# Kernel tuning notes

Hardware: AMD Instinct MI355X
Metric: run time of the kernel (lower is better)

Reference implementation:

```python
import jax, jax.numpy as jnp
import numpy as np

B, PIX_H, PIX_W = 64, 14, 14
ENC_D, DEC_D, ATT_D, EMB_D = 2048, 512, 512, 512
VOCAB, MAX_LEN = 10000, 52  # 51 decode steps


def setup_inputs() -> dict:
    key = jax.random.key(0)
    ks = jax.random.split(key, 24)
    s = 0.02
    inp = {
        'encoder_out': jax.random.normal(ks[0], (B, PIX_H, PIX_W, ENC_D), jnp.float32),
        'encoded_captions': jax.random.randint(ks[1], (B, MAX_LEN), 0, VOCAB),
        'caption_lengths': jnp.sort(jax.random.randint(ks[2], (B,), 2, MAX_LEN + 1))[::-1].at[0].set(MAX_LEN),
        # embedding (uniform -0.1..0.1 as in init_weights)
        'emb': jax.random.uniform(ks[3], (VOCAB, EMB_D), jnp.float32, -0.1, 0.1),
        # attention network
        'W_enc_att': jax.random.normal(ks[4], (ENC_D, ATT_D)) * s,
        'b_enc_att': jnp.zeros((ATT_D,)),
        'W_dec_att': jax.random.normal(ks[5], (DEC_D, ATT_D)) * s,
        'b_dec_att': jnp.zeros((ATT_D,)),
        'W_full_att': jax.random.normal(ks[6], (ATT_D, 1)) * s,
        'b_full_att': jnp.zeros((1,)),
        # init hidden state
        'W_init_h': jax.random.normal(ks[7], (ENC_D, DEC_D)) * s,
        'b_init_h': jnp.zeros((DEC_D,)),
        'W_init_c': jax.random.normal(ks[8], (ENC_D, DEC_D)) * s,
        'b_init_c': jnp.zeros((DEC_D,)),
        # gate
        'W_fbeta': jax.random.normal(ks[9], (DEC_D, ENC_D)) * s,
        'b_fbeta': jnp.zeros((ENC_D,)),
        # LSTMCell (torch gate order i,f,g,o)
        'W_ih': jax.random.normal(ks[10], (EMB_D + ENC_D, 4 * DEC_D)) * s,
        'W_hh': jax.random.normal(ks[11], (DEC_D, 4 * DEC_D)) * s,
        'b_ih': jnp.zeros((4 * DEC_D,)),
        'b_hh': jnp.zeros((4 * DEC_D,)),
        # fc (uniform -0.1..0.1, zero bias per init_weights)
        'W_fc': jax.random.uniform(ks[12], (DEC_D, VOCAB), jnp.float32, -0.1, 0.1),
        'b_fc': jnp.zeros((VOCAB,)),
    }
    return inp


def _decode(encoder_out, encoded_captions, caption_lengths, emb,
            W_enc_att, b_enc_att, W_dec_att, b_dec_att, W_full_att, b_full_att,
            W_init_h, b_init_h, W_init_c, b_init_c, W_fbeta, b_fbeta,
            W_ih, W_hh, b_ih, b_hh, W_fc, b_fc):
    bsz = encoder_out.shape[0]
    enc = encoder_out.reshape(bsz, -1, encoder_out.shape[-1])  # [B, P, ENC_D]
    embeddings = emb[encoded_captions]                          # [B, T+1, E]
    mean_enc = enc.mean(axis=1)
    h0 = mean_enc @ W_init_h + b_init_h
    c0 = mean_enc @ W_init_c + b_init_c
    att_enc = enc @ W_enc_att + b_enc_att                       # [B, P, A] precomputed
    T = encoded_captions.shape[1] - 1                           # max decode steps
    decode_len = caption_lengths - 1                            # [B]
    step_mask = jnp.arange(T)[:, None] < decode_len[None, :]    # [T, B]
    emb_seq = jnp.swapaxes(embeddings[:, :T, :], 0, 1)          # [T, B, E]

    def step(carry, xt):
        h, c = carry
        emb_t, m = xt                                           # [B,E], [B]
        # attention: 2 linears + tanh + softmax + weighted sum
        att_dec = h @ W_dec_att + b_dec_att                     # [B, A]
        e = (jnp.tanh(att_enc + att_dec[:, None, :]) @ W_full_att + b_full_att)[..., 0]  # [B, P]
        alpha = jax.nn.softmax(e, axis=-1)
        awe = jnp.einsum('bp,bpd->bd', alpha, enc)              # [B, ENC_D]
        gate = jax.nn.sigmoid(h @ W_fbeta + b_fbeta)
        awe = gate * awe
        # LSTMCell
        x = jnp.concatenate([emb_t, awe], axis=1)
        gates = x @ W_ih + h @ W_hh + (b_ih + b_hh)
        i, f, g, o = jnp.split(gates, 4, axis=1)
        c_new = jax.nn.sigmoid(f) * c + jax.nn.sigmoid(i) * jnp.tanh(g)
        h_new = jax.nn.sigmoid(o) * jnp.tanh(c_new)
        mm = m[:, None]
        h = jnp.where(mm, h_new, h)  # freeze finished rows (== batch_size_t slicing)
        c = jnp.where(mm, c_new, c)
        preds = (h @ W_fc + b_fc) * mm  # dropout = identity (eval mode)
        return (h, c), (preds, alpha * mm)

    (_, _), (preds_seq, alpha_seq) = jax.lax.scan(step, (h0, c0), (emb_seq, step_mask))
    predictions = jnp.swapaxes(preds_seq, 0, 1)  # [B, T, V]
    alphas = jnp.swapaxes(alpha_seq, 0, 1)       # [B, T, P]
    return predictions, alphas


def reference(encoder_out, encoded_captions, caption_lengths, emb,
              W_enc_att, b_enc_att, W_dec_att, b_dec_att, W_full_att, b_full_att,
              W_init_h, b_init_h, W_init_c, b_init_c, W_fbeta, b_fbeta,
              W_ih, W_hh, b_ih, b_hh, W_fc, b_fc):
    predictions, alphas = _decode(encoder_out, encoded_captions, caption_lengths, emb,
                                  W_enc_att, b_enc_att, W_dec_att, b_dec_att, W_full_att, b_full_att,
                                  W_init_h, b_init_h, W_init_c, b_init_c, W_fbeta, b_fbeta,
                                  W_ih, W_hh, b_ih, b_hh, W_fc, b_fc)
    return predictions, encoded_captions, caption_lengths - 1, alphas
```

## Files before the change

kernel.cpp:

```cpp
#include <hip/hip_runtime.h>
#include <hip/hip_bf16.h>
#include <math.h>

#define BB 64
#define NPIX 196
#define ENCD 2048
#define DECD 512
#define VOCAB_N 10000
#define MAXLEN 52
#define TT 51
#define NPADFC 10048

#define PRED_SZ   (BB * TT * VOCAB_N)
#define CAPS_SZ   (BB * MAXLEN)
#define LENS_SZ   (BB)
#define ALPHAS_OFF (PRED_SZ + CAPS_SZ + LENS_SZ)

typedef __attribute__((ext_vector_type(8))) short short8;
typedef __attribute__((ext_vector_type(4))) short short4v;
typedef __attribute__((ext_vector_type(4))) float f32x4;

__device__ __forceinline__ float fsigm(float x) {
    return 1.0f / (1.0f + __expf(-x));
}
__device__ __forceinline__ float ftanh(float x) {
    x = fminf(fmaxf(x, -15.0f), 15.0f);
    float e = __expf(2.0f * x);
    return (e - 1.0f) / (e + 1.0f);
}
__device__ __forceinline__ float bf2f(unsigned short u) {
    union { unsigned int i; float f; } v;
    v.i = ((unsigned int)u) << 16;
    return v.f;
}
__device__ __forceinline__ unsigned short f2bf(float f) {
    union { float f; unsigned int i; } v;
    v.f = f;
    unsigned int r = v.i + 0x7FFFu + ((v.i >> 16) & 1u);
    return (unsigned short)(r >> 16);
}

__global__ __launch_bounds__(256) void gemm_mfma(
    const unsigned short* __restrict__ A, int lda,
    const unsigned short* __restrict__ Wp, int Npad,
    int nkb, long slice_stride,
    float* __restrict__ C, unsigned short* __restrict__ C16, long ldc,
    const float* __restrict__ bias, int N, int act,
    const int* __restrict__ caplen, int t)
{
    const int n0 = blockIdx.x * 64;
    const int m0 = blockIdx.y * 64;
    const int kz = blockIdx.z;
    A  += (size_t)kz * nkb * 32;
    Wp += (size_t)kz * nkb * Npad * 32;
    if (C) C += (size_t)kz * slice_stride;

    const int w  = threadIdx.x >> 6;
    const int l  = threadIdx.x & 63;
    const int lr = l & 15;
    const int q  = l >> 4;

    const unsigned short* ap = A + (size_t)(m0 + 16 * w + lr) * lda + q * 8;
    const unsigned short* bp = Wp + (size_t)(n0 + lr) * 32 + q * 8;
    const size_t bstep = (size_t)Npad * 32;

    f32x4 acc[4];
#pragma unroll
    for (int i = 0; i < 4; ++i) acc[i] = (f32x4){0.f, 0.f, 0.f, 0.f};

    short8 a  = *(const short8*)ap;
    short8 b0 = *(const short8*)(bp);
    short8 b1 = *(const short8*)(bp + 512);
    short8 b2 = *(const short8*)(bp + 1024);
    short8 b3 = *(const short8*)(bp + 1536);

    for (int kb = 0; kb < nkb; ++kb) {
        const size_t nxt = (kb + 1 < nkb) ? 1 : 0;
        const unsigned short* apn = ap + nxt * 32;
        const unsigned short* bpn = bp + nxt * bstep;
        short8 an  = *(const short8*)apn;
        short8 bn0 = *(const short8*)(bpn);
        short8 bn1 = *(const short8*)(bpn + 512);
        short8 bn2 = *(const short8*)(bpn + 1024);
        short8 bn3 = *(const short8*)(bpn + 1536);
        acc[0] = __builtin_amdgcn_mfma_f32_16x16x32_bf16(a, b0, acc[0], 0, 0, 0);
        acc[1] = __builtin_amdgcn_mfma_f32_16x16x32_bf16(a, b1, acc[1], 0, 0, 0);
        acc[2] = __builtin_amdgcn_mfma_f32_16x16x32_bf16(a, b2, acc[2], 0, 0, 0);
        acc[3] = __builtin_amdgcn_mfma_f32_16x16x32_bf16(a, b3, acc[3], 0, 0, 0);
        a = an; b0 = bn0; b1 = bn1; b2 = bn2; b3 = bn3;
        ap = apn; bp = bpn;
    }

    const int r0 = q * 4;
#pragma unroll
    for (int cf = 0; cf < 4; ++cf) {
        int col = n0 + cf * 16 + lr;
        if (col >= N) continue;
        float bv = bias ? bias[col] : 0.f;
#pragma unroll
        for (int r = 0; r < 4; ++r) {
            int row = m0 + 16 * w + r0 + r;
            float v = acc[cf][r] + bv;
            if (act == 1 || (act == 2 && col < 2048)) v = fsigm(v);
            if (caplen) v *= (t < caplen[row] - 1) ? 1.f : 0.f;
            if (C16) C16[(size_t)row * ldc + col] = f2bf(v);
            else     C [(size_t)row * ldc + col] = v;
        }
    }
}

__global__ __launch_bounds__(256) void gateslstm_kernel(
    const unsigned short* __restrict__ xcatEG,
    const unsigned short* __restrict__ hprev,
    const unsigned short* __restrict__ WpLi,
    const float* __restrict__ bsum,
    const int* __restrict__ caplen, int t,
    float* __restrict__ c,
    unsigned short* __restrict__ hnext)
{
    __shared__ float gt[4][16][68];

    const int bx = blockIdx.x;
    const int nx = bx & 31;
    const int my = bx >> 5;
    const int m0 = my * 16;
    const int n0 = nx * 64;
    const int tid = threadIdx.x;
    const int ws = tid >> 6;
    const int l  = tid & 63;
    const int lr = l & 15;
    const int q  = l >> 4;

    const unsigned short* arow_x = xcatEG + (size_t)(m0 + lr) * 2560;
    const unsigned short* arow_h = hprev  + (size_t)(m0 + lr) * 512;
    const int kbase = ws * 768 + q * 8;

    const unsigned short* bp = WpLi + ((size_t)(ws * 24) * 2048 + n0 + lr) * 32 + q * 8;
    const size_t bstep = (size_t)2048 * 32;

    f32x4 acc[4];
#pragma unroll
    for (int i = 0; i < 4; ++i) acc[i] = (f32x4){0.f, 0.f, 0.f, 0.f};

#define ALOAD(kb) ({ int k0_ = kbase + (kb) * 32; \
    (k0_ < 2560) ? *(const short8*)(arow_x + k0_) \
                 : *(const short8*)(arow_h + (k0_ - 2560)); })

    short8 a  = ALOAD(0);
    short8 b0 = *(const short8*)(bp);
    short8 b1 = *(const short8*)(bp + 512);
    short8 b2 = *(const short8*)(bp + 1024);
    short8 b3 = *(const short8*)(bp + 1536);

    for (int kb = 0; kb < 24; ++kb) {
        const int kn = (kb + 1 < 24) ? kb + 1 : kb;
        const unsigned short* bpn = bp + ((kb + 1 < 24) ? bstep : 0);
        short8 an  = ALOAD(kn);
        short8 bn0 = *(const short8*)(bpn);
        short8 bn1 = *(const short8*)(bpn + 512);
        short8 bn2 = *(const short8*)(bpn + 1024);
        short8 bn3 = *(const short8*)(bpn + 1536);
        acc[0] = __builtin_amdgcn_mfma_f32_16x16x32_bf16(a, b0, acc[0], 0, 0, 0);
        acc[1] = __builtin_amdgcn_mfma_f32_16x16x32_bf16(a, b1, acc[1], 0, 0, 0);
        acc[2] = __builtin_amdgcn_mfma_f32_16x16x32_bf16(a, b2, acc[2], 0, 0, 0);
        acc[3] = __builtin_amdgcn_mfma_f32_16x16x32_bf16(a, b3, acc[3], 0, 0, 0);
        a = an; b0 = bn0; b1 = bn1; b2 = bn2; b3 = bn3;
        bp = bpn;
    }
#undef ALOAD

    const int r0 = q * 4;
#pragma unroll
    for (int cf = 0; cf < 4; ++cf)
#pragma unroll
        for (int r = 0; r < 4; ++r)
            gt[ws][r0 + r][cf * 16 + lr] = acc[cf][r];
    __syncthreads();

    const int row = tid & 15;
    const int jj  = tid >> 4;
    const int b   = m0 + row;
    const int j   = nx * 16 + jj;
    const int lc  = 4 * jj;
    float gi = bsum[j],        gf = bsum[512 + j];
    float gg = bsum[1024 + j], go = bsum[1536 + j];
#pragma unroll
    for (int s = 0; s < 4; ++s) {
        gi += gt[s][row][lc + 0];
        gf += gt[s][row][lc + 1];
        gg += gt[s][row][lc + 2];
        go += gt[s][row][lc + 3];
    }
    const int cidx = b * 512 + j;
    float cn = fsigm(gf) * c[cidx] + fsigm(gi) * ftanh(gg);
    float hn = fsigm(go) * ftanh(cn);
    bool upd = (t < caplen[b] - 1);
    if (upd) c[cidx] = cn;
    hnext[cidx] = upd ? f2bf(hn) : hprev[cidx];
}

__global__ __launch_bounds__(512) void attawe_kernel(
    const float* __restrict__ gadec,
    const unsigned short* __restrict__ attenc16,
    const unsigned short* __restrict__ enc16,
    const float* __restrict__ Wf, const float* __restrict__ bf_,
    const float* __restrict__ emb, const int* __restrict__ caps,
    const int* __restrict__ caplen, int t,
    unsigned short* __restrict__ xcatEG,
    float* __restrict__ alphas_out)
{
    int b = blockIdx.x;
    int tid = threadIdx.x;
    int lane = tid & 63, wid = tid >> 6;
    __shared__ float av[512];
    __shared__ float wv[512];
    __shared__ float es[NPIX];
    __shared__ float alpha_s[NPIX];
    __shared__ float r8[8];
    __shared__ float smax, ssum;

    av[tid] = gadec[(size_t)b * 2560 + 2048 + tid];
    wv[tid] = Wf[tid];
    __syncthreads();

    float mya[8], myw[8];
#pragma unroll
    for (int i = 0; i < 8; ++i) {
        mya[i] = av[lane * 8 + i];
        myw[i] = wv[lane * 8 + i];
    }

    float bf0 = bf_[0];
    for (int p = wid; p < NPIX; p += 8) {
        const unsigned short* ae = attenc16 + ((size_t)(b * NPIX + p)) * 512 + lane * 8;
        short8 e8 = *(const short8*)ae;
        float s = 0.f;
#pragma unroll
        for (int i = 0; i < 8; ++i)
            s += ftanh(bf2f((unsigned short)e8[i]) + mya[i]) * myw[i];
        for (int off = 32; off; off >>= 1) s += __shfl_down(s, off);
        if (lane == 0) es[p] = s + bf0;
    }
    __syncthreads();

    float v = (tid < NPIX) ? es[tid] : -1e30f;
    float m = v;
    for (int off = 32; off; off >>= 1) m = fmaxf(m, __shfl_down(m, off));
    if (lane == 0) r8[wid] = m;
    __syncthreads();
    if (tid == 0) {
        float mm = r8[0];
#pragma unroll
        for (int i = 1; i < 8; ++i) mm = fmaxf(mm, r8[i]);
        smax = mm;
    }
    __syncthreads();

    float ev = (tid < NPIX) ? __expf(v - smax) : 0.0f;
    float s = ev;
    for (int off = 32; off; off >>= 1) s += __shfl_down(s, off);
    if (lane == 0) r8[wid] = s;
    __syncthreads();
    if (tid == 0) {
        float ss = 0.f;
#pragma unroll
        for (int i = 0; i < 8; ++i) ss += r8[i];
        ssum = ss;
    }
    __syncthreads();

    float mk = (t < caplen[b] - 1) ? 1.0f : 0.0f;
    if (tid < NPIX) {
        float a = ev / ssum;
        alpha_s[tid] = a;
        alphas_out[((size_t)b * TT + t) * NPIX + tid] = a * mk;
    }
    __syncthreads();

    int d0 = tid * 4;
    const unsigned short* e = enc16 + (size_t)b * NPIX * ENCD + d0;
    float s0 = 0.f, s1 = 0.f, s2 = 0.f, s3 = 0.f;
    for (int p = 0; p < NPIX; ++p) {
        short4v v4 = *(const short4v*)(e + (size_t)p * ENCD);
        float a = alpha_s[p];
        s0 += a * bf2f((unsigned short)v4[0]);
        s1 += a * bf2f((unsigned short)v4[1]);
        s2 += a * bf2f((unsigned short)v4[2]);
        s3 += a * bf2f((unsigned short)v4[3]);
    }
    unsigned short* xr = xcatEG + (size_t)b * 2560;
    const float* gtt = gadec + (size_t)b * 2560 + d0;
    xr[512 + d0 + 0] = f2bf(s0 * gtt[0]);
    xr[512 + d0 + 1] = f2bf(s1 * gtt[1]);
    xr[512 + d0 + 2] = f2bf(s2 * gtt[2]);
    xr[512 + d0 + 3] = f2bf(s3 * gtt[3]);

    int wword = caps[b * MAXLEN + t];
    xr[tid] = f2bf(emb[(size_t)wword * 512 + tid]);
}

__global__ __launch_bounds__(256) void preds_gemm(
    const unsigned short* __restrict__ hhist,
    const unsigned short* __restrict__ WpF,
    const float* __restrict__ bfc,
    const int* __restrict__ caplen,
    float* __restrict__ out)
{
    const int n0 = blockIdx.x * 64;
    const int row0 = blockIdx.y * 64;
    const int w  = threadIdx.x >> 6;
    const int l  = threadIdx.x & 63;
    const int lr = l & 15;
    const int q  = l >> 4;

    const unsigned short* ap = hhist + (size_t)(row0 + 16 * w + lr) * 512 + q * 8;
    const unsigned short* bp = WpF + (size_t)(n0 + lr) * 32 + q * 8;
    const size_t bstep = (size_t)NPADFC * 32;

    f32x4 acc[4];
#pragma unroll
    for (int i = 0; i < 4; ++i) acc[i] = (f32x4){0.f, 0.f, 0.f, 0.f};

    short8 a  = *(const short8*)ap;
    short8 b0 = *(const short8*)(bp);
    short8 b1 = *(const short8*)(bp + 512);
    short8 b2 = *(const short8*)(bp + 1024);
    short8 b3 = *(const short8*)(bp + 1536);

    for (int kb = 0; kb < 16; ++kb) {
        const size_t nxt = (kb + 1 < 16) ? 1 : 0;
        const unsigned short* apn = ap + nxt * 32;
        const unsigned short* bpn = bp + nxt * bstep;
        short8 an  = *(const short8*)apn;
        short8 bn0 = *(const short8*)(bpn);
        short8 bn1 = *(const short8*)(bpn + 512);
        short8 bn2 = *(const short8*)(bpn + 1024);
        short8 bn3 = *(const short8*)(bpn + 1536);
        acc[0] = __builtin_amdgcn_mfma_f32_16x16x32_bf16(a, b0, acc[0], 0, 0, 0);
        acc[1] = __builtin_amdgcn_mfma_f32_16x16x32_bf16(a, b1, acc[1], 0, 0, 0);
        acc[2] = __builtin_amdgcn_mfma_f32_16x16x32_bf16(a, b2, acc[2], 0, 0, 0);
        acc[3] = __builtin_amdgcn_mfma_f32_16x16x32_bf16(a, b3, acc[3], 0, 0, 0);
        a = an; b0 = bn0; b1 = bn1; b2 = bn2; b3 = bn3;
        ap = apn; bp = bpn;
    }

    const int r0 = q * 4;
#pragma unroll
    for (int cf = 0; cf < 4; ++cf) {
        int col = n0 + cf * 16 + lr;
        if (col >= VOCAB_N) continue;
        float bv = bfc[col];
#pragma unroll
        for (int r = 0; r < 4; ++r) {
            int row = row0 + 16 * w + r0 + r;
            int tt = row >> 6, b = row & 63;
            float mk = (tt < caplen[b] - 1) ? 1.f : 0.f;
            out[((size_t)b * TT + tt) * VOCAB_N + col] = (acc[cf][r] + bv) * mk;
        }
    }
}

__global__ void pack_kernel(const float* __restrict__ W1, const float* __restrict__ W2,
                            int N1, int N2, int K1, int Npad, int mode,
                            unsigned short* __restrict__ Wp, int total)
{
    int idx = blockIdx.x * 256 + threadIdx.x;
    if (idx >= total) return;
    int kk = idx & 31;
    int r  = idx >> 5;
    int n  = r % Npad;
    int kb = r / Npad;
    int k  = kb * 32 + kk;
    float v = 0.f;
    if (mode == 0) {
        if (n < N1) v = W1[(size_t)k * N1 + n];
    } else if (mode == 1) {
        v = (n < N1) ? W1[(size_t)k * N1 + n] : W2[(size_t)k * N2 + (n - N1)];
    } else {
        v = (k < K1) ? W1[(size_t)k * N1 + n] : W2[(size_t)(k - K1) * N1 + n];
    }
    Wp[idx] = f2bf(v);
}

__global__ void packGi_kernel(const float* __restrict__ Wih,
                              const float* __restrict__ Whh,
                              unsigned short* __restrict__ Wp, int total)
{
    int idx = blockIdx.x * 256 + threadIdx.x;
    if (idx >= total) return;
    int kk = idx & 31;
    int r  = idx >> 5;
    int n  = r % 2048;
    int kb = r / 2048;
    int k  = kb * 32 + kk;
    int oc = (n & 3) * 512 + (n >> 2);
    float v = (k < 2560) ? Wih[(size_t)k * 2048 + oc]
                         : Whh[(size_t)(k - 2560) * 2048 + oc];
    Wp[idx] = f2bf(v);
}

__global__ void cast_kernel(const float* __restrict__ src,
                            unsigned short* __restrict__ dst, int n)
{
    int i = (blockIdx.x * 256 + threadIdx.x) * 4;
    if (i >= n) return;
    float4 v = *(const float4*)(src + i);
    dst[i]     = f2bf(v.x);
    dst[i + 1] = f2bf(v.y);
    dst[i + 2] = f2bf(v.z);
    dst[i + 3] = f2bf(v.w);
}

__global__ void bias_prep(const float* __restrict__ bfb, const float* __restrict__ bda,
                          const float* __restrict__ bih, const float* __restrict__ bhh,
                          float* __restrict__ bcat, float* __restrict__ bsum)
{
    int i = blockIdx.x * 256 + threadIdx.x;
    if (i < 2048) { bcat[i] = bfb[i]; bsum[i] = bih[i] + bhh[i]; }
    else if (i < 2560) bcat[i] = bda[i - 2048];
}

__global__ void mean_kernel(const float* __restrict__ enc, float* __restrict__ me)
{
    int d = blockIdx.x * 256 + threadIdx.x;
    int b = blockIdx.y;
    const float* p = enc + (size_t)b * NPIX * ENCD + d;
    float s = 0.0f;
    for (int q = 0; q < NPIX; ++q) s += p[(size_t)q * ENCD];
    me[b * ENCD + d] = s * (1.0f / 196.0f);
}

__global__ void inithc_kernel(const float* __restrict__ me,
                              const float* __restrict__ Wh, const float* __restrict__ bh,
                              const float* __restrict__ Wc, const float* __restrict__ bc,
                              unsigned short* __restrict__ hh0, float* __restrict__ c)
{
    int idx = blockIdx.x * 256 + threadIdx.x;
    int b = idx >> 9, j = idx & 511;
    const float* m = me + b * ENCD;
    float sh = bh[j], sc = bc[j];
    for (int k = 0; k < ENCD; ++k) {
        float mv = m[k];
        sh += mv * Wh[(size_t)k * DECD + j];
        sc += mv * Wc[(size_t)k * DECD + j];
    }
    hh0[idx] = f2bf(sh);
    c[idx] = sc;
}

__global__ void copy_misc(const int* __restrict__ caps, const int* __restrict__ lens,
                          float* __restrict__ out)
{
    int i = blockIdx.x * 256 + threadIdx.x;
    if (i < CAPS_SZ) out[PRED_SZ + i] = (float)caps[i];
    else if (i < CAPS_SZ + LENS_SZ) out[PRED_SZ + i] = (float)(lens[i - CAPS_SZ] - 1);
}

__global__ __launch_bounds__(256) void encatt_gemm(
    const unsigned short* __restrict__ A,
    const unsigned short* __restrict__ Wp,
    const float* __restrict__ bias,
    unsigned short* __restrict__ C16)
{
    const int n0 = blockIdx.x * 128;
    const int m0 = blockIdx.y * 128;
    const int w  = threadIdx.x >> 6;
    const int l  = threadIdx.x & 63;
    const int lr = l & 15;
    const int q  = l >> 4;

    const unsigned short* ap = A + (size_t)(m0 + 16 * w + lr) * 2048 + q * 8;
    const unsigned short* bp = Wp + (size_t)(n0 + lr) * 32 + q * 8;
    const size_t bstep = (size_t)512 * 32;

    f32x4 acc[16];
#pragma unroll
    for (int i = 0; i < 16; ++i) acc[i] = (f32x4){0.f, 0.f, 0.f, 0.f};

    short8 a0 = *(const short8*)(ap);
    short8 a1 = *(const short8*)(ap + 64 * 2048);
    short8 b[8];
#pragma unroll
    for (int nt = 0; nt < 8; ++nt) b[nt] = *(const short8*)(bp + nt * 512);

    for (int kb = 0; kb < 64; ++kb) {
        const size_t nxt = (kb + 1 < 64) ? 1 : 0;
        const unsigned short* apn = ap + nxt * 32;
        const unsigned short* bpn = bp + nxt * bstep;
        short8 an0 = *(const short8*)(apn);
        short8 an1 = *(const short8*)(apn + 64 * 2048);
        short8 bn[8];
#pragma unroll
        for (int nt = 0; nt < 8; ++nt) bn[nt] = *(const short8*)(bpn + nt * 512);
#pragma unroll
        for (int nt = 0; nt < 8; ++nt) {
            acc[nt]     = __builtin_amdgcn_mfma_f32_16x16x32_bf16(a0, b[nt], acc[nt], 0, 0, 0);
            acc[8 + nt] = __builtin_amdgcn_mfma_f32_16x16x32_bf16(a1, b[nt], acc[8 + nt], 0, 0, 0);
        }
        a0 = an0; a1 = an1;
#pragma unroll
        for (int nt = 0; nt < 8; ++nt) b[nt] = bn[nt];
        ap = apn; bp = bpn;
    }

    const int r0 = q * 4;
#pragma unroll
    for (int mt = 0; mt < 2; ++mt) {
#pragma unroll
        for (int nt = 0; nt < 8; ++nt) {
            int col = n0 + nt * 16 + lr;
            float bv = bias[col];
#pragma unroll
            for (int r = 0; r < 4; ++r) {
                int row = m0 + mt * 64 + 16 * w + r0 + r;
                C16[(size_t)row * 512 + col] = f2bf(acc[mt * 8 + nt][r] + bv);
            }
        }
    }
}

extern "C" void kernel_launch(void* const* d_in, const int* in_sizes, int n_in,
                              void* d_out, int out_size, void* d_ws, size_t ws_size,
                              hipStream_t stream)
{
    (void)in_sizes; (void)n_in; (void)out_size; (void)ws_size;
    const float* enc        = (const float*)d_in[0];
    const int*   caps       = (const int*)d_in[1];
    const int*   lens       = (const int*)d_in[2];
    const float* emb        = (const float*)d_in[3];
    const float* W_enc_att  = (const float*)d_in[4];
    const float* b_enc_att  = (const float*)d_in[5];
    const float* W_dec_att  = (const float*)d_in[6];
    const float* b_dec_att  = (const float*)d_in[7];
    const float* W_full_att = (const float*)d_in[8];
    const float* b_full_att = (const float*)d_in[9];
    const float* W_init_h   = (const float*)d_in[10];
    const float* b_init_h   = (const float*)d_in[11];
    const float* W_init_c   = (const float*)d_in[12];
    const float* b_init_c   = (const float*)d_in[13];
    const float* W_fbeta    = (const float*)d_in[14];
    const float* b_fbeta    = (const float*)d_in[15];
    const float* W_ih       = (const float*)d_in[16];
    const float* W_hh       = (const float*)d_in[17];
    const float* b_ih       = (const float*)d_in[18];
    const float* b_hh       = (const float*)d_in[19];
    const float* W_fc       = (const float*)d_in[20];
    const float* b_fc       = (const float*)d_in[21];
    float* out = (float*)d_out;

    char* p = (char*)d_ws;
    unsigned short* enc16   = (unsigned short*)p; p += (size_t)BB * NPIX * ENCD * 2;
    unsigned short* attenc16= (unsigned short*)p; p += (size_t)BB * NPIX * 512 * 2;
    unsigned short* WpLi    = (unsigned short*)p; p += (size_t)96 * 2048 * 32 * 2;
    unsigned short* WpG     = (unsigned short*)p; p += (size_t)16 * 2560 * 32 * 2;
    unsigned short* WpF     = (unsigned short*)p; p += (size_t)16 * NPADFC * 32 * 2;
    unsigned short* WpE     = (unsigned short*)p; p += (size_t)64 * 512 * 32 * 2;
    unsigned short* xcatEG  = (unsigned short*)p; p += (size_t)BB * 2560 * 2;
    unsigned short* hh      = (unsigned short*)p; p += (size_t)(TT + 1) * BB * 512 * 2;
    float* gadec  = (float*)p; p += (size_t)BB * 2560 * 4;
    float* c      = (float*)p; p += (size_t)BB * 512 * 4;
    float* me     = (float*)p; p += (size_t)BB * ENCD * 4;
    float* bcat   = (float*)p; p += 2560 * 4;
    float* bsum   = (float*)p; p += 2048 * 4;

    {
        int n = BB * NPIX * ENCD;
        cast_kernel<<<(n / 4 + 255) / 256, 256, 0, stream>>>(enc, enc16, n);
    }
    { int tot = 96 * 2048 * 32;
      packGi_kernel<<<(tot + 255) / 256, 256, 0, stream>>>(W_ih, W_hh, WpLi, tot); }
    { int tot = 16 * 2560 * 32;
      pack_kernel<<<(tot + 255) / 256, 256, 0, stream>>>(W_fbeta, W_dec_att, 2048, 512, 0, 2560, 1, WpG, tot); }
    { int tot = 16 * NPADFC * 32;
      pack_kernel<<<(tot + 255) / 256, 256, 0, stream>>>(W_fc, nullptr, VOCAB_N, 0, 0, NPADFC, 0, WpF, tot); }
    { int tot = 64 * 512 * 32;
      pack_kernel<<<(tot + 255) / 256, 256, 0, stream>>>(W_enc_att, nullptr, 512, 0, 0, 512, 0, WpE, tot); }
    bias_prep<<<10, 256, 0, stream>>>(b_fbeta, b_dec_att, b_ih, b_hh, bcat, bsum);
    mean_kernel<<<dim3(8, 64), 256, 0, stream>>>(enc, me);
    inithc_kernel<<<128, 256, 0, stream>>>(me, W_init_h, b_init_h, W_init_c, b_init_c, hh, c);
    encatt_gemm<<<dim3(4, 98), 256, 0, stream>>>(enc16, WpE, b_enc_att, attenc16);
    copy_misc<<<14, 256, 0, stream>>>(caps, lens, out);

    gemm_mfma<<<dim3(40, 1, 1), 256, 0, stream>>>(
        hh, 512, WpG, 2560, 16, 0, gadec, nullptr, 2560,
        bcat, 2560, 2, nullptr, 0);

    for (int t = 0; t < TT; ++t) {
        attawe_kernel<<<64, 512, 0, stream>>>(
            gadec, attenc16, enc16, W_full_att, b_full_att,
            emb, caps, lens, t, xcatEG, out + ALPHAS_OFF);
        gateslstm_kernel<<<128, 256, 0, stream>>>(
            xcatEG, hh + (size_t)t * BB * 512, WpLi, bsum, lens, t,
            c, hh + (size_t)(t + 1) * BB * 512);
        if (t + 1 < TT) {
            gemm_mfma<<<dim3(40, 1, 1), 256, 0, stream>>>(
                hh + (size_t)(t + 1) * BB * 512, 512, WpG, 2560, 16, 0,
                gadec, nullptr, 2560, bcat, 2560, 2, nullptr, 0);
        }
    }

    preds_gemm<<<dim3(157, TT), 256, 0, stream>>>(hh + (size_t)BB * 512, WpF, b_fc, lens, out);
}
```

Measured before the change: 3.586 ms.

## Fuse decoder-attention and gate GEMMs into attention kernel, drop per-step GEMM launch

Removes the separate per-step gemm_mfma launch that computed the f_beta gate and decoder attention projection. The decoder projection is now computed inside each attention block with a scalar dot product from a repacked bf16 weight. The gate GEMM runs in 32 extra blocks of the same launch, and the gate-times-context product moves into the LSTM kernel's A-operand load. The preds GEMM grid is also shrunk to 4 row groups, each looping over 13 time tiles. This cuts one kernel launch and one sync per decode step, at the cost of redundant scalar work per attention block and fp32 A-loads with conversion in the LSTM GEMM.

```diff
diff --git a/kernel.cpp b/kernel.cpp
--- a/kernel.cpp
+++ b/kernel.cpp
@@ -40,77 +40,10 @@
     return (unsigned short)(r >> 16);
 }
 
-__global__ __launch_bounds__(256) void gemm_mfma(
-    const unsigned short* __restrict__ A, int lda,
-    const unsigned short* __restrict__ Wp, int Npad,
-    int nkb, long slice_stride,
-    float* __restrict__ C, unsigned short* __restrict__ C16, long ldc,
-    const float* __restrict__ bias, int N, int act,
-    const int* __restrict__ caplen, int t)
-{
-    const int n0 = blockIdx.x * 64;
-    const int m0 = blockIdx.y * 64;
-    const int kz = blockIdx.z;
-    A  += (size_t)kz * nkb * 32;
-    Wp += (size_t)kz * nkb * Npad * 32;
-    if (C) C += (size_t)kz * slice_stride;
-
-    const int w  = threadIdx.x >> 6;
-    const int l  = threadIdx.x & 63;
-    const int lr = l & 15;
-    const int q  = l >> 4;
-
-    const unsigned short* ap = A + (size_t)(m0 + 16 * w + lr) * lda + q * 8;
-    const unsigned short* bp = Wp + (size_t)(n0 + lr) * 32 + q * 8;
-    const size_t bstep = (size_t)Npad * 32;
-
-    f32x4 acc[4];
-#pragma unroll
-    for (int i = 0; i < 4; ++i) acc[i] = (f32x4){0.f, 0.f, 0.f, 0.f};
-
-    short8 a  = *(const short8*)ap;
-    short8 b0 = *(const short8*)(bp);
-    short8 b1 = *(const short8*)(bp + 512);
-    short8 b2 = *(const short8*)(bp + 1024);
-    short8 b3 = *(const short8*)(bp + 1536);
-
-    for (int kb = 0; kb < nkb; ++kb) {
-        const size_t nxt = (kb + 1 < nkb) ? 1 : 0;
-        const unsigned short* apn = ap + nxt * 32;
-        const unsigned short* bpn = bp + nxt * bstep;
-        short8 an  = *(const short8*)apn;
-        short8 bn0 = *(const short8*)(bpn);
-        short8 bn1 = *(const short8*)(bpn + 512);
-        short8 bn2 = *(const short8*)(bpn + 1024);
-        short8 bn3 = *(const short8*)(bpn + 1536);
-        acc[0] = __builtin_amdgcn_mfma_f32_16x16x32_bf16(a, b0, acc[0], 0, 0, 0);
-        acc[1] = __builtin_amdgcn_mfma_f32_16x16x32_bf16(a, b1, acc[1], 0, 0, 0);
-        acc[2] = __builtin_amdgcn_mfma_f32_16x16x32_bf16(a, b2, acc[2], 0, 0, 0);
-        acc[3] = __builtin_amdgcn_mfma_f32_16x16x32_bf16(a, b3, acc[3], 0, 0, 0);
-        a = an; b0 = bn0; b1 = bn1; b2 = bn2; b3 = bn3;
-        ap = apn; bp = bpn;
-    }
-
-    const int r0 = q * 4;
-#pragma unroll
-    for (int cf = 0; cf < 4; ++cf) {
-        int col = n0 + cf * 16 + lr;
-        if (col >= N) continue;
-        float bv = bias ? bias[col] : 0.f;
-#pragma unroll
-        for (int r = 0; r < 4; ++r) {
-            int row = m0 + 16 * w + r0 + r;
-            float v = acc[cf][r] + bv;
-            if (act == 1 || (act == 2 && col < 2048)) v = fsigm(v);
-            if (caplen) v *= (t < caplen[row] - 1) ? 1.f : 0.f;
-            if (C16) C16[(size_t)row * ldc + col] = f2bf(v);
-            else     C [(size_t)row * ldc + col] = v;
-        }
-    }
-}
-
 __global__ __launch_bounds__(256) void gateslstm_kernel(
-    const unsigned short* __restrict__ xcatEG,
+    const unsigned short* __restrict__ xemb,
+    const float* __restrict__ aweF,
+    const float* __restrict__ gateF,
     const unsigned short* __restrict__ hprev,
     const unsigned short* __restrict__ WpLi,
     const float* __restrict__ bsum,
@@ -131,9 +64,32 @@
     const int lr = l & 15;
     const int q  = l >> 4;
 
-    const unsigned short* arow_x = xcatEG + (size_t)(m0 + lr) * 2560;
-    const unsigned short* arow_h = hprev  + (size_t)(m0 + lr) * 512;
+    const unsigned short* arow_e = xemb  + (size_t)(m0 + lr) * 512;
+    const float*          arow_a = aweF  + (size_t)(m0 + lr) * 2048;
+    const float*          arow_g = gateF + (size_t)(m0 + lr) * 2048;
+    const unsigned short* arow_h = hprev + (size_t)(m0 + lr) * 512;
     const int kbase = ws * 768 + q * 8;
+
+    auto aload = [&](int kb) -> short8 {
+        int k0 = kbase + kb * 32;
+        if (k0 < 512) {
+            return *(const short8*)(arow_e + k0);
+        } else if (k0 < 2560) {
+            int d = k0 - 512;
+            float4 a0 = *(const float4*)(arow_a + d);
+            float4 a1 = *(const float4*)(arow_a + d + 4);
+            float4 g0 = *(const float4*)(arow_g + d);
+            float4 g1 = *(const float4*)(arow_g + d + 4);
+            short8 r;
+            r[0] = (short)f2bf(a0.x * g0.x); r[1] = (short)f2bf(a0.y * g0.y);
+            r[2] = (short)f2bf(a0.z * g0.z); r[3] = (short)f2bf(a0.w * g0.w);
+            r[4] = (short)f2bf(a1.x * g1.x); r[5] = (short)f2bf(a1.y * g1.y);
+            r[6] = (short)f2bf(a1.z * g1.z); r[7] = (short)f2bf(a1.w * g1.w);
+            return r;
+        } else {
+            return *(const short8*)(arow_h + (k0 - 2560));
+        }
+    };
 
     const unsigned short* bp = WpLi + ((size_t)(ws * 24) * 2048 + n0 + lr) * 32 + q * 8;
     const size_t bstep = (size_t)2048 * 32;
@@ -142,11 +98,7 @@
 #pragma unroll
     for (int i = 0; i < 4; ++i) acc[i] = (f32x4){0.f, 0.f, 0.f, 0.f};
 
-#define ALOAD(kb) ({ int k0_ = kbase + (kb) * 32; \
-    (k0_ < 2560) ? *(const short8*)(arow_x + k0_) \
-                 : *(const short8*)(arow_h + (k0_ - 2560)); })
-
-    short8 a  = ALOAD(0);
+    short8 a  = aload(0);
     short8 b0 = *(const short8*)(bp);
     short8 b1 = *(const short8*)(bp + 512);
     short8 b2 = *(const short8*)(bp + 1024);
@@ -155,7 +107,7 @@
     for (int kb = 0; kb < 24; ++kb) {
         const int kn = (kb + 1 < 24) ? kb + 1 : kb;
         const unsigned short* bpn = bp + ((kb + 1 < 24) ? bstep : 0);
-        short8 an  = ALOAD(kn);
+        short8 an  = aload(kn);
         short8 bn0 = *(const short8*)(bpn);
         short8 bn1 = *(const short8*)(bpn + 512);
         short8 bn2 = *(const short8*)(bpn + 1024);
@@ -167,7 +119,6 @@
         a = an; b0 = bn0; b1 = bn1; b2 = bn2; b3 = bn3;
         bp = bpn;
     }
-#undef ALOAD
 
     const int r0 = q * 4;
 #pragma unroll
@@ -200,18 +151,71 @@
 }
 
 __global__ __launch_bounds__(512) void attawe_kernel(
-    const float* __restrict__ gadec,
+    const unsigned short* __restrict__ hT,
+    const unsigned short* __restrict__ WdK,
+    const float* __restrict__ bda,
+    const unsigned short* __restrict__ WpB,
+    const float* __restrict__ bfb,
     const unsigned short* __restrict__ attenc16,
     const unsigned short* __restrict__ enc16,
     const float* __restrict__ Wf, const float* __restrict__ bf_,
     const float* __restrict__ emb, const int* __restrict__ caps,
     const int* __restrict__ caplen, int t,
-    unsigned short* __restrict__ xcatEG,
+    unsigned short* __restrict__ xemb,
+    float* __restrict__ aweF,
+    float* __restrict__ gateF,
     float* __restrict__ alphas_out)
 {
-    int b = blockIdx.x;
-    int tid = threadIdx.x;
-    int lane = tid & 63, wid = tid >> 6;
+    const int bx = blockIdx.x;
+    const int tid = threadIdx.x;
+
+    if (bx >= 64) {
+        const int nx = bx - 64;
+        const int w  = tid >> 6;
+        const int l  = tid & 63;
+        const int lr = l & 15;
+        const int q  = l >> 4;
+        const int wr = w & 3;
+        const int ch = w >> 2;
+        const int n0 = nx * 64 + ch * 32;
+
+        const unsigned short* ap = hT + (size_t)(16 * wr + lr) * 512 + q * 8;
+        const unsigned short* bp = WpB + (size_t)(n0 + lr) * 32 + q * 8;
+        const size_t bstep = (size_t)2048 * 32;
+
+        f32x4 acc0 = (f32x4){0.f,0.f,0.f,0.f}, acc1 = (f32x4){0.f,0.f,0.f,0.f};
+        short8 a  = *(const short8*)ap;
+        short8 b0 = *(const short8*)(bp);
+        short8 b1 = *(const short8*)(bp + 512);
+        for (int kb = 0; kb < 16; ++kb) {
+            const size_t nxt = (kb + 1 < 16) ? 1 : 0;
+            const unsigned short* apn = ap + nxt * 32;
+            const unsigned short* bpn = bp + nxt * bstep;
+            short8 an  = *(const short8*)apn;
+            short8 bn0 = *(const short8*)(bpn);
+            short8 bn1 = *(const short8*)(bpn + 512);
+            acc0 = __builtin_amdgcn_mfma_f32_16x16x32_bf16(a, b0, acc0, 0, 0, 0);
+            acc1 = __builtin_amdgcn_mfma_f32_16x16x32_bf16(a, b1, acc1, 0, 0, 0);
+            a = an; b0 = bn0; b1 = bn1; ap = apn; bp = bpn;
+        }
+        const int r0 = q * 4;
+#pragma unroll
+        for (int cf = 0; cf < 2; ++cf) {
+            int col = n0 + cf * 16 + lr;
+            float bv = bfb[col];
+            f32x4 ac = cf ? acc1 : acc0;
+#pragma unroll
+            for (int r = 0; r < 4; ++r) {
+                int row = 16 * wr + r0 + r;
+                gateF[(size_t)row * 2048 + col] = fsigm(ac[r] + bv);
+            }
+        }
+        return;
+    }
+
+    const int b = bx;
+    const int lane = tid & 63, wid = tid >> 6;
+    __shared__ float h_sh[512];
     __shared__ float av[512];
     __shared__ float wv[512];
     __shared__ float es[NPIX];
@@ -219,8 +223,18 @@
     __shared__ float r8[8];
     __shared__ float smax, ssum;
 
-    av[tid] = gadec[(size_t)b * 2560 + 2048 + tid];
+    h_sh[tid] = bf2f(hT[(size_t)b * 512 + tid]);
     wv[tid] = Wf[tid];
+    __syncthreads();
+
+    float aa = 0.f;
+    for (int kk = 0; kk < 64; ++kk) {
+        short8 w8 = *(const short8*)(WdK + ((size_t)(kk * 512 + tid)) * 8);
+#pragma unroll
+        for (int u = 0; u < 8; ++u)
+            aa += h_sh[kk * 8 + u] * bf2f((unsigned short)w8[u]);
+    }
+    av[tid] = aa + bda[tid];
     __syncthreads();
 
     float mya[8], myw[8];
@@ -288,15 +302,10 @@
         s2 += a * bf2f((unsigned short)v4[2]);
         s3 += a * bf2f((unsigned short)v4[3]);
     }
-    unsigned short* xr = xcatEG + (size_t)b * 2560;
-    const float* gtt = gadec + (size_t)b * 2560 + d0;
-    xr[512 + d0 + 0] = f2bf(s0 * gtt[0]);
-    xr[512 + d0 + 1] = f2bf(s1 * gtt[1]);
-    xr[512 + d0 + 2] = f2bf(s2 * gtt[2]);
-    xr[512 + d0 + 3] = f2bf(s3 * gtt[3]);
+    *(float4*)(aweF + (size_t)b * 2048 + d0) = make_float4(s0, s1, s2, s3);
 
     int wword = caps[b * MAXLEN + t];
-    xr[tid] = f2bf(emb[(size_t)wword * 512 + tid]);
+    xemb[(size_t)b * 512 + tid] = f2bf(emb[(size_t)wword * 512 + tid]);
 }
 
 __global__ __launch_bounds__(256) void preds_gemm(
@@ -307,55 +316,61 @@
     float* __restrict__ out)
 {
     const int n0 = blockIdx.x * 64;
-    const int row0 = blockIdx.y * 64;
+    const int my = blockIdx.y;
     const int w  = threadIdx.x >> 6;
     const int l  = threadIdx.x & 63;
     const int lr = l & 15;
     const int q  = l >> 4;
-
-    const unsigned short* ap = hhist + (size_t)(row0 + 16 * w + lr) * 512 + q * 8;
-    const unsigned short* bp = WpF + (size_t)(n0 + lr) * 32 + q * 8;
     const size_t bstep = (size_t)NPADFC * 32;
 
-    f32x4 acc[4];
-#pragma unroll
-    for (int i = 0; i < 4; ++i) acc[i] = (f32x4){0.f, 0.f, 0.f, 0.f};
-
-    short8 a  = *(const short8*)ap;
-    short8 b0 = *(const short8*)(bp);
-    short8 b1 = *(const short8*)(bp + 512);
-    short8 b2 = *(const short8*)(bp + 1024);
-    short8 b3 = *(const short8*)(bp + 1536);
-
-    for (int kb = 0; kb < 16; ++kb) {
-        const size_t nxt = (kb + 1 < 16) ? 1 : 0;
-        const unsigned short* apn = ap + nxt * 32;
-        const unsigned short* bpn = bp + nxt * bstep;
-        short8 an  = *(const short8*)apn;
-        short8 bn0 = *(const short8*)(bpn);
-        short8 bn1 = *(const short8*)(bpn + 512);
-        short8 bn2 = *(const short8*)(bpn + 1024);
-        short8 bn3 = *(const short8*)(bpn + 1536);
-        acc[0] = __builtin_amdgcn_mfma_f32_16x16x32_bf16(a, b0, acc[0], 0, 0, 0);
-        acc[1] = __builtin_amdgcn_mfma_f32_16x16x32_bf16(a, b1, acc[1], 0, 0, 0);
-        acc[2] = __builtin_amdgcn_mfma_f32_16x16x32_bf16(a, b2, acc[2], 0, 0, 0);
-        acc[3] = __builtin_amdgcn_mfma_f32_16x16x32_bf16(a, b3, acc[3], 0, 0, 0);
-        a = an; b0 = bn0; b1 = bn1; b2 = bn2; b3 = bn3;
-        ap = apn; bp = bpn;
-    }
-
-    const int r0 = q * 4;
-#pragma unroll
-    for (int cf = 0; cf < 4; ++cf) {
-        int col = n0 + cf * 16 + lr;
-        if (col >= VOCAB_N) continue;
-        float bv = bfc[col];
-#pragma unroll
-        for (int r = 0; r < 4; ++r) {
-            int row = row0 + 16 * w + r0 + r;
-            int tt = row >> 6, b = row & 63;
-            float mk = (tt < caplen[b] - 1) ? 1.f : 0.f;
-            out[((size_t)b * TT + tt) * VOCAB_N + col] = (acc[cf][r] + bv) * mk;
+    for (int mt = 0; mt < 13; ++mt) {
+        int tile = my * 13 + mt;
+        if (tile >= TT) break;
+        int row0 = tile * 64;
+
+        const unsigned short* ap = hhist + (size_t)(row0 + 16 * w + lr) * 512 + q * 8;
+        const unsigned short* bp = WpF + (size_t)(n0 + lr) * 32 + q * 8;
+
+        f32x4 acc[4];
+#pragma unroll
+        for (int i = 0; i < 4; ++i) acc[i] = (f32x4){0.f, 0.f, 0.f, 0.f};
+
+        short8 a  = *(const short8*)ap;
+        short8 b0 = *(const short8*)(bp);
+        short8 b1 = *(const short8*)(bp + 512);
+        short8 b2 = *(const short8*)(bp + 1024);
+        short8 b3 = *(const short8*)(bp + 1536);
+
+        for (int kb = 0; kb < 16; ++kb) {
+            const size_t nxt = (kb + 1 < 16) ? 1 : 0;
+            const unsigned short* apn = ap + nxt * 32;
+            const unsigned short* bpn = bp + nxt * bstep;
+            short8 an  = *(const short8*)apn;
+            short8 bn0 = *(const short8*)(bpn);
+            short8 bn1 = *(const short8*)(bpn + 512);
+            short8 bn2 = *(const short8*)(bpn + 1024);
+            short8 bn3 = *(const short8*)(bpn + 1536);
+            acc[0] = __builtin_amdgcn_mfma_f32_16x16x32_bf16(a, b0, acc[0], 0, 0, 0);
+            acc[1] = __builtin_amdgcn_mfma_f32_16x16x32_bf16(a, b1, acc[1], 0, 0, 0);
+            acc[2] = __builtin_amdgcn_mfma_f32_16x16x32_bf16(a, b2, acc[2], 0, 0, 0);
+            acc[3] = __builtin_amdgcn_mfma_f32_16x16x32_bf16(a, b3, acc[3], 0, 0, 0);
+            a = an; b0 = bn0; b1 = bn1; b2 = bn2; b3 = bn3;
+            ap = apn; bp = bpn;
+        }
+
+        const int r0 = q * 4;
+#pragma unroll
+        for (int cf = 0; cf < 4; ++cf) {
+            int col = n0 + cf * 16 + lr;
+            if (col >= VOCAB_N) continue;
+            float bv = bfc[col];
+#pragma unroll
+            for (int r = 0; r < 4; ++r) {
+                int row = row0 + 16 * w + r0 + r;
+                int tt = row >> 6, b = row & 63;
+                float mk = (tt < caplen[b] - 1) ? 1.f : 0.f;
+                out[((size_t)b * TT + tt) * VOCAB_N + col] = (acc[cf][r] + bv) * mk;
+            }
         }
     }
 }
@@ -399,6 +414,19 @@
     Wp[idx] = f2bf(v);
 }
 
+__global__ void packDK_kernel(const float* __restrict__ Wda,
+                              unsigned short* __restrict__ Wp, int total)
+{
+    int idx = blockIdx.x * 256 + threadIdx.x;
+    if (idx >= total) return;
+    int u  = idx & 7;
+    int r  = idx >> 3;
+    int n  = r & 511;
+    int kk = r >> 9;
+    int k  = kk * 8 + u;
+    Wp[idx] = f2bf(Wda[(size_t)k * 512 + n]);
+}
+
 __global__ void cast_kernel(const float* __restrict__ src,
                             unsigned short* __restrict__ dst, int n)
 {
@@ -411,13 +439,11 @@
     dst[i + 3] = f2bf(v.w);
 }
 
-__global__ void bias_prep(const float* __restrict__ bfb, const float* __restrict__ bda,
-                          const float* __restrict__ bih, const float* __restrict__ bhh,
-                          float* __restrict__ bcat, float* __restrict__ bsum)
+__global__ void bsum_prep(const float* __restrict__ bih, const float* __restrict__ bhh,
+                          float* __restrict__ bsum)
 {
     int i = blockIdx.x * 256 + threadIdx.x;
-    if (i < 2048) { bcat[i] = bfb[i]; bsum[i] = bih[i] + bhh[i]; }
-    else if (i < 2560) bcat[i] = bda[i - 2048];
+    if (i < 2048) bsum[i] = bih[i] + bhh[i];
 }
 
 __global__ void mean_kernel(const float* __restrict__ enc, float* __restrict__ me)
@@ -552,15 +578,16 @@
     unsigned short* enc16   = (unsigned short*)p; p += (size_t)BB * NPIX * ENCD * 2;
     unsigned short* attenc16= (unsigned short*)p; p += (size_t)BB * NPIX * 512 * 2;
     unsigned short* WpLi    = (unsigned short*)p; p += (size_t)96 * 2048 * 32 * 2;
-    unsigned short* WpG     = (unsigned short*)p; p += (size_t)16 * 2560 * 32 * 2;
     unsigned short* WpF     = (unsigned short*)p; p += (size_t)16 * NPADFC * 32 * 2;
     unsigned short* WpE     = (unsigned short*)p; p += (size_t)64 * 512 * 32 * 2;
-    unsigned short* xcatEG  = (unsigned short*)p; p += (size_t)BB * 2560 * 2;
+    unsigned short* WpB     = (unsigned short*)p; p += (size_t)16 * 2048 * 32 * 2;
+    unsigned short* WdK     = (unsigned short*)p; p += (size_t)64 * 512 * 8 * 2;
+    unsigned short* xemb    = (unsigned short*)p; p += (size_t)BB * 512 * 2;
     unsigned short* hh      = (unsigned short*)p; p += (size_t)(TT + 1) * BB * 512 * 2;
-    float* gadec  = (float*)p; p += (size_t)BB * 2560 * 4;
+    float* aweF   = (float*)p; p += (size_t)BB * 2048 * 4;
+    float* gateF  = (float*)p; p += (size_t)BB * 2048 * 4;
     float* c      = (float*)p; p += (size_t)BB * 512 * 4;
     float* me     = (float*)p; p += (size_t)BB * ENCD * 4;
-    float* bcat   = (float*)p; p += 2560 * 4;
     float* bsum   = (float*)p; p += 2048 * 4;
 
     {
@@ -569,35 +596,29 @@
     }
     { int tot = 96 * 2048 * 32;
       packGi_kernel<<<(tot + 255) / 256, 256, 0, stream>>>(W_ih, W_hh, WpLi, tot); }
-    { int tot = 16 * 2560 * 32;
-      pack_kernel<<<(tot + 255) / 256, 256, 0, stream>>>(W_fbeta, W_dec_att, 2048, 512, 0, 2560, 1, WpG, tot); }
     { int tot = 16 * NPADFC * 32;
       pack_kernel<<<(tot + 255) / 256, 256, 0, stream>>>(W_fc, nullptr, VOCAB_N, 0, 0, NPADFC, 0, WpF, tot); }
     { int tot = 64 * 512 * 32;
       pack_kernel<<<(tot + 255) / 256, 256, 0, stream>>>(W_enc_att, nullptr, 512, 0, 0, 512, 0, WpE, tot); }
-    bias_prep<<<10, 256, 0, stream>>>(b_fbeta, b_dec_att, b_ih, b_hh, bcat, bsum);
+    { int tot = 16 * 2048 * 32;
+      pack_kernel<<<(tot + 255) / 256, 256, 0, stream>>>(W_fbeta, nullptr, 2048, 0, 0, 2048, 0, WpB, tot); }
+    { int tot = 64 * 512 * 8;
+      packDK_kernel<<<(tot + 255) / 256, 256, 0, stream>>>(W_dec_att, WdK, tot); }
+    bsum_prep<<<8, 256, 0, stream>>>(b_ih, b_hh, bsum);
     mean_kernel<<<dim3(8, 64), 256, 0, stream>>>(enc, me);
     inithc_kernel<<<128, 256, 0, stream>>>(me, W_init_h, b_init_h, W_init_c, b_init_c, hh, c);
     encatt_gemm<<<dim3(4, 98), 256, 0, stream>>>(enc16, WpE, b_enc_att, attenc16);
     copy_misc<<<14, 256, 0, stream>>>(caps, lens, out);
 
-    gemm_mfma<<<dim3(40, 1, 1), 256, 0, stream>>>(
-        hh, 512, WpG, 2560, 16, 0, gadec, nullptr, 2560,
-        bcat, 2560, 2, nullptr, 0);
-
     for (int t = 0; t < TT; ++t) {
-        attawe_kernel<<<64, 512, 0, stream>>>(
-            gadec, attenc16, enc16, W_full_att, b_full_att,
-            emb, caps, lens, t, xcatEG, out + ALPHAS_OFF);
+        attawe_kernel<<<96, 512, 0, stream>>>(
+            hh + (size_t)t * BB * 512, WdK, b_dec_att, WpB, b_fbeta,
+            attenc16, enc16, W_full_att, b_full_att,
+            emb, caps, lens, t, xemb, aweF, gateF, out + ALPHAS_OFF);
         gateslstm_kernel<<<128, 256, 0, stream>>>(
-            xcatEG, hh + (size_t)t * BB * 512, WpLi, bsum, lens, t,
+            xemb, aweF, gateF, hh + (size_t)t * BB * 512, WpLi, bsum, lens, t,
             c, hh + (size_t)(t + 1) * BB * 512);
-        if (t + 1 < TT) {
-            gemm_mfma<<<dim3(40, 1, 1), 256, 0, stream>>>(
-                hh + (size_t)(t + 1) * BB * 512, 512, WpG, 2560, 16, 0,
-                gadec, nullptr, 2560, bcat, 2560, 2, nullptr, 0);
-        }
-    }
-
-    preds_gemm<<<dim3(157, TT), 256, 0, stream>>>(hh + (size_t)BB * 512, WpF, b_fc, lens, out);
-}
+    }
+
+    preds_gemm<<<dim3(157, 4), 256, 0, stream>>>(hh + (size_t)BB * 512, WpF, b_fc, lens, out);
+}
```

Result: slower. 4.324 ms (+20.6%).
